# Kernel optimization log

Hardware: AMD Instinct MI355X
Metric: run time of the kernel (lower is better)

## Reference

```python
import jax, jax.numpy as jnp
import numpy as np

B, D, C = 1024, 512, 100000
S, M = 64.0, 0.1
EPS = 1e-12  # torch F.normalize eps


def setup_inputs() -> dict:
    key = jax.random.key(0)
    k1, k2, k3 = jax.random.split(key, 3)
    inputs = jax.random.normal(k1, (B, D), dtype=jnp.float32)
    labels = jax.random.randint(k2, (B,), 0, C, dtype=jnp.int64)
    weight = jax.random.normal(k3, (C, D), dtype=jnp.float32)
    return {"inputs": inputs, "labels": labels, "weight": weight}


def _l2norm(x):
    # matches F.normalize: x / max(||x||, eps)
    n = jnp.sqrt(jnp.sum(x * x, axis=-1, keepdims=True))
    return x / jnp.maximum(n, EPS)


def reference(inputs, labels, weight):
    # cosine similarity: [B, C]
    cos_theta = jnp.clip(_l2norm(inputs) @ _l2norm(weight).T, -1.0, 1.0)
    theta = jnp.arccos(cos_theta)
    # add margin m only at the label column (one-hot scatter without materializing one_hot)
    rows = jnp.arange(theta.shape[0])
    theta_m = theta.at[rows, labels].add(M)
    logits = S * jnp.cos(theta_m)
    # cross-entropy (mean reduction)
    logp = jax.nn.log_softmax(logits, axis=-1)
    loss = -jnp.mean(logp[rows, labels])
    return loss
```

## Files before the change

### kernel.cpp

```cpp
#include <hip/hip_runtime.h>
#include <hip/hip_bf16.h>
#include <stdint.h>

#define DIM 512
#define NROWS 1024
#define NCLS 100000
#define NCLS_PAD 100032
#define SCALE_S 64.0f
#define NBN 192
#define NSTRIPE ((NCLS + 63) / 64)
#define S_LOG2E 92.332482616893662f

typedef __attribute__((ext_vector_type(8))) __bf16 bf16x8;
typedef __attribute__((ext_vector_type(4))) float f32x4;

__device__ __forceinline__ unsigned short f2bf(float x) {
  __hip_bfloat16 h = __float2bfloat16(x);
  union { __hip_bfloat16 h; unsigned short u; } v; v.h = h; return v.u;
}
__device__ __forceinline__ unsigned pack2(float a, float b) {
  return ((unsigned)f2bf(b) << 16) | (unsigned)f2bf(a);
}
__device__ __forceinline__ void async_ld16(const void* g, void* l) {
  __builtin_amdgcn_global_load_lds((const __attribute__((address_space(1))) void*)g,
                                   (__attribute__((address_space(3))) void*)l, 16, 0, 0);
}

__global__ void prep_a(const float* __restrict__ X, unsigned short* __restrict__ A16,
                       float* __restrict__ xnorm) {
  const int row = blockIdx.x;
  const int lane = threadIdx.x;
  const float4* xp = (const float4*)(X + (size_t)row * DIM);
  float4 v0 = xp[lane];
  float4 v1 = xp[lane + 64];
  float ss = v0.x*v0.x + v0.y*v0.y + v0.z*v0.z + v0.w*v0.w
           + v1.x*v1.x + v1.y*v1.y + v1.z*v1.z + v1.w*v1.w;
  #pragma unroll
  for (int m = 1; m < 64; m <<= 1) ss += __shfl_xor(ss, m);
  const float nrm = sqrtf(ss);
  const float inv = 1.0f / fmaxf(nrm, 1e-12f);
  if (lane == 0) xnorm[row] = nrm;
  unsigned short* ap = A16 + (size_t)row * DIM;
  *(uint2*)(ap + lane * 4)       = make_uint2(pack2(v0.x*inv, v0.y*inv), pack2(v0.z*inv, v0.w*inv));
  *(uint2*)(ap + 256 + lane * 4) = make_uint2(pack2(v1.x*inv, v1.y*inv), pack2(v1.z*inv, v1.w*inv));
}

__global__ void prep_w(const float* __restrict__ Wg, unsigned short* __restrict__ W16) {
  const int row = blockIdx.x * 4 + (threadIdx.x >> 6);
  const int lane = threadIdx.x & 63;
  unsigned short* op = W16 + (size_t)row * DIM;
  if (row >= NCLS) {
    *(uint4*)((char*)op + lane * 16) = make_uint4(0, 0, 0, 0);
    return;
  }
  const float4* xp = (const float4*)(Wg + (size_t)row * DIM);
  float4 v0 = xp[lane];
  float4 v1 = xp[lane + 64];
  float ss = v0.x*v0.x + v0.y*v0.y + v0.z*v0.z + v0.w*v0.w
           + v1.x*v1.x + v1.y*v1.y + v1.z*v1.z + v1.w*v1.w;
  #pragma unroll
  for (int m = 1; m < 64; m <<= 1) ss += __shfl_xor(ss, m);
  const float inv = 1.0f / fmaxf(sqrtf(ss), 1e-12f);
  *(uint2*)(op + lane * 4)       = make_uint2(pack2(v0.x*inv, v0.y*inv), pack2(v0.z*inv, v0.w*inv));
  *(uint2*)(op + 256 + lane * 4) = make_uint2(pack2(v1.x*inv, v1.y*inv), pack2(v1.z*inv, v1.w*inv));
}


__device__ __forceinline__ void stage_w(const char* W16g, char* wldsb, int buf, int ktp,
                                        int tcol0, int wave, int lane) {
  #pragma unroll
  for (int it = 0; it < 2; ++it) {
    const int d = (wave * 2 + it) * 1024 + lane * 16;
    const int c = d >> 7;
    const int b = d & 127;
    async_ld16(W16g + ((size_t)(tcol0 + c) * 1024 + ktp * 128 + (b ^ ((c & 7) << 4))),
               wldsb + buf * 8192 + (wave * 2 + it) * 1024);
  }
}

template<int KT>
__device__ __forceinline__ void mfma_phase(const char* wldsb, const bf16x8 (&af)[8][2][2],
                                           f32x4 (&acc)[2][4], int lr, int lg) {
  const char* wb = wldsb + KT * 8192;
  bf16x8 bfr[2][4];
  #pragma unroll
  for (int kh = 0; kh < 2; ++kh)
    #pragma unroll
    for (int ni = 0; ni < 4; ++ni) {
      const int bc = ni * 16 + lr;
      const int o = (bc * 128 + kh * 64 + lg * 16) ^ ((bc & 7) << 4);
      bfr[kh][ni] = *(const bf16x8*)(wb + o);
    }
  #pragma unroll
  for (int kh = 0; kh < 2; ++kh)
    #pragma unroll
    for (int mi = 0; mi < 2; ++mi)
      #pragma unroll
      for (int ni = 0; ni < 4; ++ni)
        acc[mi][ni] = __builtin_amdgcn_mfma_f32_16x16x32_bf16(af[KT][kh][mi], bfr[kh][ni], acc[mi][ni], 0, 0, 0);
}

#define PHASE(KT, VMT)                                                              \
  do {                                                                              \
    if ((KT) < 2) {                                                                 \
      stage_w(W16g, wldsb, ((KT) + 6) & 7, (KT) + 6, col0, wave, lane);             \
      asm volatile("s_waitcnt vmcnt(12)" ::: "memory");                             \
    } else if (has_next) {                                                          \
      stage_w(W16g, wldsb, ((KT) + 6) & 7, (KT) - 2, ncol0, wave, lane);            \
      asm volatile("s_waitcnt vmcnt(12)" ::: "memory");                             \
    } else {                                                                        \
      asm volatile("s_waitcnt vmcnt(" #VMT ")" ::: "memory");                       \
    }                                                                               \
    __builtin_amdgcn_s_barrier();                                                   \
    mfma_phase<(KT)>(wldsb, af, acc, lr, lg);                                       \
  } while (0)

__global__ __launch_bounds__(256, 2) void gemm_lse2(
    const unsigned short* __restrict__ A16, const unsigned short* __restrict__ W16,
    float* __restrict__ part_s) {
  __shared__ char wlds[8 * 8192];
  char* wldsb = wlds;
  const char* W16g = (const char*)W16;

  const int tid = threadIdx.x;
  const int lane = tid & 63;
  const int wave = tid >> 6;
  const int lr = lane & 15, lg = lane >> 4;
  const int bid = blockIdx.x;
  const int mblk = (bid >> 3) & 7;
  const int nblk = ((bid >> 6) << 3) + (bid & 7);

  bf16x8 af[8][2][2];
  {
    const char* Ab = (const char*)A16 + (size_t)(mblk * 128 + wave * 32) * 1024;
    #pragma unroll
    for (int kt = 0; kt < 8; ++kt)
      #pragma unroll
      for (int kh = 0; kh < 2; ++kh)
        #pragma unroll
        for (int mi = 0; mi < 2; ++mi)
          af[kt][kh][mi] = *(const bf16x8*)(Ab + (size_t)(mi * 16 + lr) * 1024 + kt * 128 + kh * 64 + lg * 16);
  }
  #pragma unroll
  for (int kt = 0; kt < 8; ++kt)
    #pragma unroll
    for (int kh = 0; kh < 2; ++kh)
      #pragma unroll
      for (int mi = 0; mi < 2; ++mi)
        asm volatile("" : "+a"(af[kt][kh][mi]));

  f32x4 acc[2][4];
  #pragma unroll
  for (int mi = 0; mi < 2; ++mi)
    #pragma unroll
    for (int ni = 0; ni < 4; ++ni) acc[mi][ni] = f32x4{0.f, 0.f, 0.f, 0.f};
  float srow[2][4];
  #pragma unroll
  for (int mi = 0; mi < 2; ++mi)
    #pragma unroll
    for (int r = 0; r < 4; ++r) srow[mi][r] = 0.f;

  {
    const int c0 = nblk * 64;
    #pragma unroll
    for (int pk = 0; pk < 6; ++pk) stage_w(W16g, wldsb, pk, pk, c0, wave, lane);
  }

  for (int s = nblk; s < NSTRIPE; s += NBN) {
    const int col0 = s * 64;
    const int ncol0 = (s + NBN) * 64;
    const bool has_next = (s + NBN) < NSTRIPE;

    PHASE(0, 12); PHASE(1, 12); PHASE(2, 10); PHASE(3, 8);
    PHASE(4, 6);  PHASE(5, 4);  PHASE(6, 2);  PHASE(7, 0);

    #pragma unroll
    for (int mi = 0; mi < 2; ++mi)
      #pragma unroll
      for (int ni = 0; ni < 4; ++ni) {
        const bool ok = (col0 + ni * 16 + lr) < NCLS;
        #pragma unroll
        for (int r = 0; r < 4; ++r) {
          float c = fminf(1.f, fmaxf(-1.f, acc[mi][ni][r]));
          srow[mi][r] += ok ? exp2f(fmaf(c, S_LOG2E, -S_LOG2E)) : 0.f;
          acc[mi][ni][r] = 0.f;
        }
      }
  }

  #pragma unroll
  for (int mi = 0; mi < 2; ++mi)
    #pragma unroll
    for (int r = 0; r < 4; ++r) {
      float v = srow[mi][r];
      v += __shfl_xor(v, 1); v += __shfl_xor(v, 2);
      v += __shfl_xor(v, 4); v += __shfl_xor(v, 8);
      if (lr == 0)
        part_s[(size_t)nblk * NROWS + mblk * 128 + wave * 32 + mi * 16 + lg * 4 + r] = v;
    }
}

__global__ void finalize_kernel(const float* __restrict__ X, const int* __restrict__ labels,
                                const float* __restrict__ Wg, const float* __restrict__ xnorm,
                                const float* __restrict__ part_s, float* __restrict__ rowloss) {
  const int row = blockIdx.x;
  const int lane = threadIdx.x;
  const int lbl = labels[row];
  const float4* xp = (const float4*)(X + (size_t)row * DIM);
  const float4* wp = (const float4*)(Wg + (size_t)lbl * DIM);
  float dot = 0.f, wss = 0.f;
  #pragma unroll
  for (int i = 0; i < 2; ++i) {
    float4 xv = xp[lane + 64 * i];
    float4 wv = wp[lane + 64 * i];
    dot += xv.x*wv.x + xv.y*wv.y + xv.z*wv.z + xv.w*wv.w;
    wss += wv.x*wv.x + wv.y*wv.y + wv.z*wv.z + wv.w*wv.w;
  }
  float psum = 0.f;
  #pragma unroll
  for (int i = 0; i < NBN / 64; ++i)
    psum += part_s[(size_t)(lane + 64 * i) * NROWS + row];
  #pragma unroll
  for (int m = 1; m < 64; m <<= 1) {
    dot += __shfl_xor(dot, m); wss += __shfl_xor(wss, m); psum += __shfl_xor(psum, m);
  }
  if (lane == 0) {
    float c = dot / (fmaxf(xnorm[row], 1e-12f) * fmaxf(sqrtf(wss), 1e-12f));
    c = fminf(1.f, fmaxf(-1.f, c));
    const float cm = 0.99500416527802576610f;
    const float sn = 0.09983341664682815230f;
    float unmod = SCALE_S * c;
    float modv  = SCALE_S * (c * cm - sqrtf(fmaxf(0.f, 1.f - c * c)) * sn);
    float stot = psum - __expf(unmod - SCALE_S) + __expf(modv - SCALE_S);
    stot = fmaxf(stot, 1e-37f);
    rowloss[row] = (logf(stot) + SCALE_S) - modv;
  }
}

__global__ void reduce_kernel(const float* __restrict__ rowloss, float* __restrict__ out) {
  const int tid = threadIdx.x;
  float s = 0.f;
  #pragma unroll
  for (int i = 0; i < 4; ++i) s += rowloss[tid + i * 256];
  #pragma unroll
  for (int m = 1; m < 64; m <<= 1) s += __shfl_xor(s, m);
  __shared__ float wsum[4];
  if ((tid & 63) == 0) wsum[tid >> 6] = s;
  __syncthreads();
  if (tid == 0) out[0] = (wsum[0] + wsum[1] + wsum[2] + wsum[3]) * (1.0f / NROWS);
}

extern "C" void kernel_launch(void* const* d_in, const int* in_sizes, int n_in,
                              void* d_out, int out_size, void* d_ws, size_t ws_size,
                              hipStream_t stream) {
  const float* X      = (const float*)d_in[0];
  const int*   labels = (const int*)d_in[1];
  const float* Wg     = (const float*)d_in[2];
  float* out = (float*)d_out;
  char* ws = (char*)d_ws;
  unsigned short* A16 = (unsigned short*)ws;
  unsigned short* W16 = (unsigned short*)(ws + 1048576);
  float* part_s  = (float*)(ws + 103481344);
  float* xnorm   = (float*)(ws + 104267776);
  float* rowloss = (float*)(ws + 104271872);

  prep_a<<<NROWS, 64, 0, stream>>>(X, A16, xnorm);
  prep_w<<<NCLS_PAD / 4, 256, 0, stream>>>(Wg, W16);
  gemm_lse2<<<NBN * 8, 256, 0, stream>>>(A16, W16, part_s);
  finalize_kernel<<<NROWS, 64, 0, stream>>>(X, labels, Wg, xnorm, part_s, rowloss);
  reduce_kernel<<<1, 256, 0, stream>>>(rowloss, out);
}
```

Measured before the change: 178.6 us.

## Stream A fragments per k-phase instead of holding all in AGPRs

The GEMM no longer preloads all eight k-slices of the A operand into accumulator registers for the whole kernel. It double-buffers two k-slices and reloads the next slice from global memory (expected to hit in L2) at the start of each phase, with the vmcnt waits adjusted for the extra loads. It also drops the per-column bounds mask in the softmax-sum epilogue, relying on the zeroed padded W rows. The aim is to cut register pressure and simplify the epilogue. In exchange it adds repeated global loads of A per stripe, and the padded columns now add a small extra term to the sum.

```diff
diff --git a/kernel.cpp b/kernel.cpp
--- a/kernel.cpp
+++ b/kernel.cpp
@@ -8,7 +8,7 @@
 #define NCLS_PAD 100032
 #define SCALE_S 64.0f
 #define NBN 192
-#define NSTRIPE ((NCLS + 63) / 64)
+#define NST ((NCLS + 63) / 64)
 #define S_LOG2E 92.332482616893662f
 
 typedef __attribute__((ext_vector_type(8))) __bf16 bf16x8;
@@ -67,7 +67,7 @@
 
 
 __device__ __forceinline__ void stage_w(const char* W16g, char* wldsb, int buf, int ktp,
-                                        int tcol0, int wave, int lane) {
+                                        long tcol0, int wave, int lane) {
   #pragma unroll
   for (int it = 0; it < 2; ++it) {
     const int d = (wave * 2 + it) * 1024 + lane * 16;
@@ -78,8 +78,18 @@
   }
 }
 
+__device__ __forceinline__ void lda(bf16x8 (&dst)[2][2], const char* Ab, int kt,
+                                    int lr, int lg) {
+  #pragma unroll
+  for (int kh = 0; kh < 2; ++kh)
+    #pragma unroll
+    for (int mi = 0; mi < 2; ++mi)
+      dst[kh][mi] = *(const bf16x8*)(Ab + (size_t)(mi * 16 + lr) * 1024
+                                        + kt * 128 + kh * 64 + lg * 16);
+}
+
 template<int KT>
-__device__ __forceinline__ void mfma_phase(const char* wldsb, const bf16x8 (&af)[8][2][2],
+__device__ __forceinline__ void mfma_phase(const char* wldsb, const bf16x8 (&afc)[2][2],
                                            f32x4 (&acc)[2][4], int lr, int lg) {
   const char* wb = wldsb + KT * 8192;
   bf16x8 bfr[2][4];
@@ -97,25 +107,26 @@
     for (int mi = 0; mi < 2; ++mi)
       #pragma unroll
       for (int ni = 0; ni < 4; ++ni)
-        acc[mi][ni] = __builtin_amdgcn_mfma_f32_16x16x32_bf16(af[KT][kh][mi], bfr[kh][ni], acc[mi][ni], 0, 0, 0);
+        acc[mi][ni] = __builtin_amdgcn_mfma_f32_16x16x32_bf16(afc[kh][mi], bfr[kh][ni], acc[mi][ni], 0, 0, 0);
 }
 
 #define PHASE(KT, VMT)                                                              \
   do {                                                                              \
+    lda(af[((KT) + 1) & 1], Ab, ((KT) + 1) & 7, lr, lg);                            \
     if ((KT) < 2) {                                                                 \
       stage_w(W16g, wldsb, ((KT) + 6) & 7, (KT) + 6, col0, wave, lane);             \
-      asm volatile("s_waitcnt vmcnt(12)" ::: "memory");                             \
+      asm volatile("s_waitcnt vmcnt(8)" ::: "memory");                              \
     } else if (has_next) {                                                          \
       stage_w(W16g, wldsb, ((KT) + 6) & 7, (KT) - 2, ncol0, wave, lane);            \
-      asm volatile("s_waitcnt vmcnt(12)" ::: "memory");                             \
+      asm volatile("s_waitcnt vmcnt(8)" ::: "memory");                              \
     } else {                                                                        \
       asm volatile("s_waitcnt vmcnt(" #VMT ")" ::: "memory");                       \
     }                                                                               \
     __builtin_amdgcn_s_barrier();                                                   \
-    mfma_phase<(KT)>(wldsb, af, acc, lr, lg);                                       \
+    mfma_phase<(KT)>(wldsb, af[(KT) & 1], acc, lr, lg);                             \
   } while (0)
 
-__global__ __launch_bounds__(256, 2) void gemm_lse2(
+__global__ __launch_bounds__(256, 2) void gemm_lse4(
     const unsigned short* __restrict__ A16, const unsigned short* __restrict__ W16,
     float* __restrict__ part_s) {
   __shared__ char wlds[8 * 8192];
@@ -130,24 +141,7 @@
   const int mblk = (bid >> 3) & 7;
   const int nblk = ((bid >> 6) << 3) + (bid & 7);
 
-  bf16x8 af[8][2][2];
-  {
-    const char* Ab = (const char*)A16 + (size_t)(mblk * 128 + wave * 32) * 1024;
-    #pragma unroll
-    for (int kt = 0; kt < 8; ++kt)
-      #pragma unroll
-      for (int kh = 0; kh < 2; ++kh)
-        #pragma unroll
-        for (int mi = 0; mi < 2; ++mi)
-          af[kt][kh][mi] = *(const bf16x8*)(Ab + (size_t)(mi * 16 + lr) * 1024 + kt * 128 + kh * 64 + lg * 16);
-  }
-  #pragma unroll
-  for (int kt = 0; kt < 8; ++kt)
-    #pragma unroll
-    for (int kh = 0; kh < 2; ++kh)
-      #pragma unroll
-      for (int mi = 0; mi < 2; ++mi)
-        asm volatile("" : "+a"(af[kt][kh][mi]));
+  const char* Ab = (const char*)A16 + (size_t)(mblk * 128 + wave * 32) * 1024;
 
   f32x4 acc[2][4];
   #pragma unroll
@@ -160,32 +154,34 @@
     #pragma unroll
     for (int r = 0; r < 4; ++r) srow[mi][r] = 0.f;
 
+  bf16x8 af[2][2][2];
+
+  lda(af[0], Ab, 0, lr, lg);
   {
-    const int c0 = nblk * 64;
+    const long c0 = (long)nblk * 64;
     #pragma unroll
     for (int pk = 0; pk < 6; ++pk) stage_w(W16g, wldsb, pk, pk, c0, wave, lane);
   }
 
-  for (int s = nblk; s < NSTRIPE; s += NBN) {
-    const int col0 = s * 64;
-    const int ncol0 = (s + NBN) * 64;
-    const bool has_next = (s + NBN) < NSTRIPE;
-
-    PHASE(0, 12); PHASE(1, 12); PHASE(2, 10); PHASE(3, 8);
-    PHASE(4, 6);  PHASE(5, 4);  PHASE(6, 2);  PHASE(7, 0);
+  for (int s = nblk; s < NST; s += NBN) {
+    const long col0 = (long)s * 64;
+    const long ncol0 = (long)(s + NBN) * 64;
+    const bool has_next = (s + NBN) < NST;
+    asm volatile("" : "+v"(Ab));
+
+    PHASE(0, 8); PHASE(1, 8); PHASE(2, 6); PHASE(3, 4);
+    PHASE(4, 4); PHASE(5, 4); PHASE(6, 4); PHASE(7, 4);
 
     #pragma unroll
     for (int mi = 0; mi < 2; ++mi)
       #pragma unroll
-      for (int ni = 0; ni < 4; ++ni) {
-        const bool ok = (col0 + ni * 16 + lr) < NCLS;
+      for (int ni = 0; ni < 4; ++ni)
         #pragma unroll
         for (int r = 0; r < 4; ++r) {
           float c = fminf(1.f, fmaxf(-1.f, acc[mi][ni][r]));
-          srow[mi][r] += ok ? exp2f(fmaf(c, S_LOG2E, -S_LOG2E)) : 0.f;
+          srow[mi][r] += exp2f(fmaf(c, S_LOG2E, -S_LOG2E));
           acc[mi][ni][r] = 0.f;
         }
-      }
   }
 
   #pragma unroll
@@ -266,7 +262,7 @@
 
   prep_a<<<NROWS, 64, 0, stream>>>(X, A16, xnorm);
   prep_w<<<NCLS_PAD / 4, 256, 0, stream>>>(Wg, W16);
-  gemm_lse2<<<NBN * 8, 256, 0, stream>>>(A16, W16, part_s);
+  gemm_lse4<<<NBN * 8, 256, 0, stream>>>(A16, W16, part_s);
   finalize_kernel<<<NROWS, 64, 0, stream>>>(X, labels, Wg, xnorm, part_s, rowloss);
   reduce_kernel<<<1, 256, 0, stream>>>(rowloss, out);
 }
```

Result: slower. 264.2 us (+47.9%).
